# Performance work log

Measured on AMD Instinct MI355X. Metric: run time of the kernel, lower is better.

Reference implementation:

```python
import jax, jax.numpy as jnp
import numpy as np

N = 16384
K = 4096  # codebook_size
D = 512   # embedding_dim
COMMITMENT_COST = 0.25


def setup_inputs() -> dict:
    key = jax.random.key(0)
    kz, kc = jax.random.split(key)
    z = jax.random.normal(kz, (N, D), dtype=jnp.float32)
    # nn.Embedding weight init: uniform(-1/K, 1/K)
    codebook = jax.random.uniform(kc, (K, D), dtype=jnp.float32,
                                  minval=-1.0 / K, maxval=1.0 / K)
    return {"z": z, "codebook": codebook}


def reference(z, codebook):
    # squared L2 distances: [N, K]
    dists = (jnp.sum(z * z, axis=1, keepdims=True)
             + jnp.sum(codebook * codebook, axis=1)
             - 2.0 * jnp.matmul(z, codebook.T))
    idx = jnp.argmin(dists, axis=1)                 # [N]
    z_q = codebook[idx]                             # gather == one-hot @ codebook
    # straight-through estimator
    z_q_ste = z + jax.lax.stop_gradient(z_q - z)
    commitment_loss = jnp.mean((jax.lax.stop_gradient(z) - z_q) ** 2)
    codebook_loss = jnp.mean((z - jax.lax.stop_gradient(z_q)) ** 2)
    loss = codebook_loss + COMMITMENT_COST * commitment_loss
    encoding_indices = idx[:, None]                 # [N, 1] to match torch shape
    return (z_q_ste, encoding_indices, loss)
```

## Files before the change

kernel.cpp:

```cpp
#include <hip/hip_runtime.h>
#include <math.h>

#define N_ROWS 16384
#define K_CODES 4096
#define D_DIM 512
#define NCHUNK 8
#define KCHUNK (K_CODES / NCHUNK)
#define MARGIN 2.5e-3f

typedef unsigned int uint32;
typedef unsigned short u16t;
typedef __attribute__((ext_vector_type(8))) short short8;
typedef __attribute__((ext_vector_type(4))) float f32x4;

__device__ __forceinline__ float fmul_(float a, float b) { return __fmul_rn(a, b); }
__device__ __forceinline__ float fadd_(float a, float b) { return __fadd_rn(a, b); }

__device__ __forceinline__ u16t f2bf(float x) {
    uint32 u = __float_as_uint(x);
    return (u16t)((u + 0x7fffu + ((u >> 16) & 1u)) >> 16);
}
__device__ __forceinline__ float bf2f(u16t b) {
    return __uint_as_float(((uint32)b) << 16);
}

__global__ void rownorm_cvt_kernel(const float* __restrict__ src, int nrows,
                                   float* __restrict__ out,
                                   u16t* __restrict__ bf) {
    int gid = blockIdx.x * blockDim.x + threadIdx.x;
    int row = gid >> 2;
    int blk = gid & 3;
    if (row >= nrows) return;
    const size_t base = (size_t)row * D_DIM + blk * 128;
    const float4* p = (const float4*)(src + base);
    float4 v0 = p[0], v1 = p[1];
    if (bf) {
        ushort4 o0, o1;
        o0.x = f2bf(v0.x); o0.y = f2bf(v0.y); o0.z = f2bf(v0.z); o0.w = f2bf(v0.w);
        o1.x = f2bf(v1.x); o1.y = f2bf(v1.y); o1.z = f2bf(v1.z); o1.w = f2bf(v1.w);
        *(ushort4*)(bf + base) = o0;
        *(ushort4*)(bf + base + 4) = o1;
    }
    float r0 = fmul_(v0.x, v0.x), r1 = fmul_(v0.y, v0.y);
    float r2 = fmul_(v0.z, v0.z), r3 = fmul_(v0.w, v0.w);
    float r4 = fmul_(v1.x, v1.x), r5 = fmul_(v1.y, v1.y);
    float r6 = fmul_(v1.z, v1.z), r7 = fmul_(v1.w, v1.w);
#pragma unroll
    for (int i = 1; i < 16; i++) {
        float4 w0 = p[2 * i], w1 = p[2 * i + 1];
        if (bf) {
            ushort4 o0, o1;
            o0.x = f2bf(w0.x); o0.y = f2bf(w0.y); o0.z = f2bf(w0.z); o0.w = f2bf(w0.w);
            o1.x = f2bf(w1.x); o1.y = f2bf(w1.y); o1.z = f2bf(w1.z); o1.w = f2bf(w1.w);
            *(ushort4*)(bf + base + i * 8) = o0;
            *(ushort4*)(bf + base + i * 8 + 4) = o1;
        }
        r0 = fadd_(r0, fmul_(w0.x, w0.x));
        r1 = fadd_(r1, fmul_(w0.y, w0.y));
        r2 = fadd_(r2, fmul_(w0.z, w0.z));
        r3 = fadd_(r3, fmul_(w0.w, w0.w));
        r4 = fadd_(r4, fmul_(w1.x, w1.x));
        r5 = fadd_(r5, fmul_(w1.y, w1.y));
        r6 = fadd_(r6, fmul_(w1.z, w1.z));
        r7 = fadd_(r7, fmul_(w1.w, w1.w));
    }
    float s = fadd_(fadd_(fadd_(r0, r1), fadd_(r2, r3)),
                    fadd_(fadd_(r4, r5), fadd_(r6, r7)));
    float u = __shfl_down(s, 1, 64);
    float t = fadd_(s, u);
    float w = __shfl_down(t, 2, 64);
    float tot = fadd_(t, w);
    if (blk == 0) out[row] = tot;
}

#define STS 136

__global__ __launch_bounds__(256) void score_gemm_kernel(
    const u16t* __restrict__ zb, const u16t* __restrict__ cbb,
    const float* __restrict__ cnorm, u16t* __restrict__ scores) {
    __shared__ alignas(16) u16t Ab[128 * 32];
    __shared__ alignas(16) u16t Bb[128 * 32];
    __shared__ alignas(16) u16t stile[64 * STS];

    const int t = threadIdx.x;
    const int id = blockIdx.x;
    const int xcd = id & 7, q = id >> 3;
    const int bx = ((xcd & 3) << 1) | (q >> 6);
    const int by = ((xcd >> 2) << 6) | (q & 63);
    const int row0 = by * 128, k0 = bx * KCHUNK;
    const int w = t >> 6, lane = t & 63;
    const int wx = w & 1, wy = w >> 1;
    const int l15 = lane & 15, quad = lane >> 4;

    for (int kt = 0; kt < 4; kt++) {
        f32x4 acc[4][4];
#pragma unroll
        for (int i = 0; i < 4; i++)
#pragma unroll
            for (int j = 0; j < 4; j++) acc[i][j] = (f32x4){0.f, 0.f, 0.f, 0.f};

        for (int dt = 0; dt < 16; dt++) {
            __syncthreads();
#pragma unroll
            for (int qq = 0; qq < 2; qq++) {
                int s = qq * 256 + t;
                const u16t* ga = zb + (size_t)(row0 + (s >> 2)) * D_DIM + dt * 32 + (s & 3) * 8;
                __builtin_amdgcn_global_load_lds(
                    (const __attribute__((address_space(1))) void*)ga,
                    (__attribute__((address_space(3))) void*)((char*)Ab + qq * 4096 + w * 1024),
                    16, 0, 0);
                const u16t* gb = cbb + (size_t)(k0 + kt * 128 + (s >> 2)) * D_DIM + dt * 32 + (s & 3) * 8;
                __builtin_amdgcn_global_load_lds(
                    (const __attribute__((address_space(1))) void*)gb,
                    (__attribute__((address_space(3))) void*)((char*)Bb + qq * 4096 + w * 1024),
                    16, 0, 0);
            }
            __syncthreads();
            short8 a[4], b[4];
#pragma unroll
            for (int i = 0; i < 4; i++)
                a[i] = *(const short8*)((char*)Ab + (wy * 64 + i * 16 + l15) * 64 + quad * 16);
#pragma unroll
            for (int j = 0; j < 4; j++)
                b[j] = *(const short8*)((char*)Bb + (wx * 64 + j * 16 + l15) * 64 + quad * 16);
#pragma unroll
            for (int i = 0; i < 4; i++)
#pragma unroll
                for (int j = 0; j < 4; j++)
                    acc[i][j] = __builtin_amdgcn_mfma_f32_16x16x32_bf16(a[i], b[j], acc[i][j], 0, 0, 0);
        }
#pragma unroll
        for (int h = 0; h < 2; h++) {
            if (wy == h) {
#pragma unroll
                for (int j = 0; j < 4; j++) {
                    int cl = wx * 64 + j * 16 + l15;
                    float cn = cnorm[k0 + kt * 128 + cl];
#pragma unroll
                    for (int i = 0; i < 4; i++) {
#pragma unroll
                        for (int r = 0; r < 4; r++) {
                            int rl2 = i * 16 + quad * 4 + r;
                            float s = fmaf(-2.f, acc[i][j][r], cn);
                            stile[rl2 * STS + cl] = f2bf(s);
                        }
                    }
                }
            }
            __syncthreads();
            for (int idx = t; idx < 64 * 16; idx += 256) {
                int rr = idx >> 4, seg = idx & 15;
                short8 v = *(const short8*)&stile[rr * STS + seg * 8];
                *(short8*)(scores + (size_t)(row0 + h * 64 + rr) * K_CODES
                           + k0 + kt * 128 + seg * 8) = v;
            }
            __syncthreads();
        }
    }
}

__global__ __launch_bounds__(256) void scan_refine_wave_kernel(
    const u16t* __restrict__ scores,
    const float* __restrict__ z, const float* __restrict__ cb,
    const float* __restrict__ zz, const float* __restrict__ cnorm,
    float* __restrict__ out_zq, float* __restrict__ out_idx,
    float* __restrict__ rowsum) {
    const int t = threadIdx.x;
    const int w = t >> 6, lane = t & 63;
    const int row = blockIdx.x * 4 + w;

    const u16t* srow = scores + (size_t)row * K_CODES;
    short8 sv[8];
#pragma unroll
    for (int p = 0; p < 8; p++)
        sv[p] = *(const short8*)(srow + p * 512 + lane * 8);

    float m = 3.4e38f;
#pragma unroll
    for (int p = 0; p < 8; p++)
#pragma unroll
        for (int e = 0; e < 8; e++)
            m = fminf(m, bf2f((u16t)sv[p][e]));
#pragma unroll
    for (int off = 1; off < 64; off <<= 1)
        m = fminf(m, __shfl_xor(m, off, 64));
    const float thr = m + MARGIN;

    const float* zr = z + (size_t)row * D_DIM;
    float4 z0 = *(const float4*)(zr + lane * 8);
    float4 z1 = *(const float4*)(zr + lane * 8 + 4);
    const float zzr = zz[row];

    float bv = 3.4e38f;
    int bi = 0x7fffffff;
#pragma unroll
    for (int p = 0; p < 8; p++) {
        uint32 lm = 0u;
#pragma unroll
        for (int e = 0; e < 8; e++)
            if (bf2f((u16t)sv[p][e]) <= thr) lm |= (1u << e);
        unsigned long long act = __ballot(lm != 0u);
        while (act) {
            int src = __ffsll(act) - 1;
            act &= act - 1;
            uint32 mb = (uint32)__shfl((int)lm, src, 64);
            while (mb) {
                int e = __ffs(mb) - 1;
                mb &= mb - 1;
                int k = p * 512 + src * 8 + e;
                const float* cr = cb + (size_t)k * D_DIM;
                float4 c0 = *(const float4*)(cr + lane * 8);
                float4 c1 = *(const float4*)(cr + lane * 8 + 4);
                float d = fmul_(z0.x, c0.x);
                d = fmaf(z0.y, c0.y, d); d = fmaf(z0.z, c0.z, d); d = fmaf(z0.w, c0.w, d);
                d = fmaf(z1.x, c1.x, d); d = fmaf(z1.y, c1.y, d);
                d = fmaf(z1.z, c1.z, d); d = fmaf(z1.w, c1.w, d);
#pragma unroll
                for (int off = 1; off < 64; off <<= 1)
                    d = fadd_(d, __shfl_xor(d, off, 64));
                float dist = fmaf(-2.f, d, fadd_(zzr, cnorm[k]));
                if (dist < bv || (dist == bv && k < bi)) { bv = dist; bi = k; }
            }
        }
    }
    const float* cq = cb + (size_t)bi * D_DIM;
    float4 c0 = *(const float4*)(cq + lane * 8);
    float4 c1 = *(const float4*)(cq + lane * 8 + 4);
    float4 o0, o1;
    o0.x = fadd_(z0.x, __fsub_rn(c0.x, z0.x));
    o0.y = fadd_(z0.y, __fsub_rn(c0.y, z0.y));
    o0.z = fadd_(z0.z, __fsub_rn(c0.z, z0.z));
    o0.w = fadd_(z0.w, __fsub_rn(c0.w, z0.w));
    o1.x = fadd_(z1.x, __fsub_rn(c1.x, z1.x));
    o1.y = fadd_(z1.y, __fsub_rn(c1.y, z1.y));
    o1.z = fadd_(z1.z, __fsub_rn(c1.z, z1.z));
    o1.w = fadd_(z1.w, __fsub_rn(c1.w, z1.w));
    float* orow = out_zq + (size_t)row * D_DIM + lane * 8;
    *(float4*)(orow) = o0;
    *(float4*)(orow + 4) = o1;
    float dx0 = z0.x - c0.x, dy0 = z0.y - c0.y, dz0 = z0.z - c0.z, dw0 = z0.w - c0.w;
    float dx1 = z1.x - c1.x, dy1 = z1.y - c1.y, dz1 = z1.z - c1.z, dw1 = z1.w - c1.w;
    float s = dx0 * dx0 + dy0 * dy0 + dz0 * dz0 + dw0 * dw0
            + dx1 * dx1 + dy1 * dy1 + dz1 * dz1 + dw1 * dw1;
#pragma unroll
    for (int off = 32; off; off >>= 1) s += __shfl_down(s, off, 64);
    if (lane == 0) {
        rowsum[row] = s;
        out_idx[row] = (float)bi;
    }
}

__global__ void loss_kernel(const float* __restrict__ rowsum,
                            float* __restrict__ out_loss) {
    __shared__ float sm[256];
    float s = 0.f;
    for (int i = threadIdx.x; i < N_ROWS; i += 256) s += rowsum[i];
    sm[threadIdx.x] = s;
    __syncthreads();
    for (int st = 128; st; st >>= 1) {
        if (threadIdx.x < st) sm[threadIdx.x] += sm[threadIdx.x + st];
        __syncthreads();
    }
    if (threadIdx.x == 0)
        *out_loss = 1.25f * sm[0] / (float)(N_ROWS * D_DIM);
}

#define BM 128
#define BN 128
#define BK 16
#define TM 8
#define TN 8

__global__ __launch_bounds__(256, 4) void vq_argmin_kernel(
    const float* __restrict__ z, const float* __restrict__ cb,
    const float* __restrict__ zz, const float* __restrict__ cnorm,
    float* __restrict__ pval, int* __restrict__ pidx) {
    __shared__ float As[BK][BM + 4];
    __shared__ float Bs[BK][BN + 4];
    __shared__ float rv[BM][17];
    __shared__ int   ri[BM][17];

    const int bx = blockIdx.x;
    const int by = blockIdx.y;
    const int row0 = by * BM;
    const int k0 = bx * KCHUNK;
    const int t = threadIdx.x;
    const int tx = t & 15;
    const int ty = t >> 4;

    float minv[TM];
    int   mini[TM];
#pragma unroll
    for (int i = 0; i < TM; i++) { minv[i] = 3.4e38f; mini[i] = 0; }
    float zrow[TM];
#pragma unroll
    for (int i = 0; i < TM; i++) zrow[i] = zz[row0 + ty * TM + i];
    const int sr = t >> 1;
    const int sdq = (t & 1) * 8;

    for (int kt = 0; kt < KCHUNK / BN; kt++) {
        const int col0 = k0 + kt * BN;
        float acc[TM][TN];
#pragma unroll
        for (int i = 0; i < TM; i++)
#pragma unroll
            for (int j = 0; j < TN; j++) acc[i][j] = 0.f;
        for (int dt = 0; dt < D_DIM; dt += BK) {
            {
                const float* src = z + (size_t)(row0 + sr) * D_DIM + dt + sdq;
                float4 v0 = *(const float4*)(src);
                float4 v1 = *(const float4*)(src + 4);
                As[sdq + 0][sr] = v0.x; As[sdq + 1][sr] = v0.y;
                As[sdq + 2][sr] = v0.z; As[sdq + 3][sr] = v0.w;
                As[sdq + 4][sr] = v1.x; As[sdq + 5][sr] = v1.y;
                As[sdq + 6][sr] = v1.z; As[sdq + 7][sr] = v1.w;
                const float* srcb = cb + (size_t)(col0 + sr) * D_DIM + dt + sdq;
                float4 w0 = *(const float4*)(srcb);
                float4 w1 = *(const float4*)(srcb + 4);
                Bs[sdq + 0][sr] = w0.x; Bs[sdq + 1][sr] = w0.y;
                Bs[sdq + 2][sr] = w0.z; Bs[sdq + 3][sr] = w0.w;
                Bs[sdq + 4][sr] = w1.x; Bs[sdq + 5][sr] = w1.y;
                Bs[sdq + 6][sr] = w1.z; Bs[sdq + 7][sr] = w1.w;
            }
            __syncthreads();
#pragma unroll
            for (int d = 0; d < BK; d++) {
                float a[TM], b[TN];
#pragma unroll
                for (int i = 0; i < TM; i++) a[i] = As[d][ty * TM + i];
#pragma unroll
                for (int j = 0; j < TN; j++) b[j] = Bs[d][tx * TN + j];
#pragma unroll
                for (int i = 0; i < TM; i++)
#pragma unroll
                    for (int j = 0; j < TN; j++)
                        acc[i][j] = fmaf(a[i], b[j], acc[i][j]);
            }
            __syncthreads();
        }
#pragma unroll
        for (int j = 0; j < TN; j++) {
            const int col = col0 + tx * TN + j;
            const float cn = cnorm[col];
#pragma unroll
            for (int i = 0; i < TM; i++) {
                float s1 = fadd_(zrow[i], cn);
                float s = fmaf(-2.f, acc[i][j], s1);
                if (s < minv[i]) { minv[i] = s; mini[i] = col; }
            }
        }
    }
#pragma unroll
    for (int i = 0; i < TM; i++) {
        rv[ty * TM + i][tx] = minv[i];
        ri[ty * TM + i][tx] = mini[i];
    }
    __syncthreads();
    if (t < BM) {
        float bv = rv[t][0];
        int   bi = ri[t][0];
#pragma unroll
        for (int x = 1; x < 16; x++) {
            float v = rv[t][x]; int ii = ri[t][x];
            if (v < bv || (v == bv && ii < bi)) { bv = v; bi = ii; }
        }
        pval[(size_t)(row0 + t) * NCHUNK + bx] = bv;
        pidx[(size_t)(row0 + t) * NCHUNK + bx] = bi;
    }
}

__global__ void finalize_kernel(const float* __restrict__ z,
                                const float* __restrict__ cb,
                                const float* __restrict__ pval,
                                const int* __restrict__ pidx,
                                float* __restrict__ out_zq,
                                float* __restrict__ out_idx,
                                float* __restrict__ rowsum) {
    int row = (blockIdx.x * blockDim.x + threadIdx.x) >> 6;
    int lane = threadIdx.x & 63;
    if (row >= N_ROWS) return;
    float bv = pval[(size_t)row * NCHUNK];
    int   bi = pidx[(size_t)row * NCHUNK];
#pragma unroll
    for (int c = 1; c < NCHUNK; c++) {
        float v = pval[(size_t)row * NCHUNK + c];
        int  ii = pidx[(size_t)row * NCHUNK + c];
        if (v < bv || (v == bv && ii < bi)) { bv = v; bi = ii; }
    }
    const float4* zr = (const float4*)(z + (size_t)row * D_DIM);
    const float4* cr = (const float4*)(cb + (size_t)bi * D_DIM);
    float4* orow = (float4*)(out_zq + (size_t)row * D_DIM);
    float s = 0.f;
#pragma unroll
    for (int i = 0; i < 2; i++) {
        float4 zv = zr[i * 64 + lane];
        float4 cv = cr[i * 64 + lane];
        float4 o;
        o.x = fadd_(zv.x, __fsub_rn(cv.x, zv.x));
        o.y = fadd_(zv.y, __fsub_rn(cv.y, zv.y));
        o.z = fadd_(zv.z, __fsub_rn(cv.z, zv.z));
        o.w = fadd_(zv.w, __fsub_rn(cv.w, zv.w));
        orow[i * 64 + lane] = o;
        float dx = zv.x - cv.x, dy = zv.y - cv.y;
        float dz = zv.z - cv.z, dw = zv.w - cv.w;
        s += dx * dx + dy * dy + dz * dz + dw * dw;
    }
#pragma unroll
    for (int off = 32; off; off >>= 1) s += __shfl_down(s, off, 64);
    if (lane == 0) {
        rowsum[row] = s;
        out_idx[row] = (float)bi;
    }
}

extern "C" void kernel_launch(void* const* d_in, const int* in_sizes, int n_in,
                              void* d_out, int out_size, void* d_ws, size_t ws_size,
                              hipStream_t stream) {
    const float* z  = (const float*)d_in[0];
    const float* cb = (const float*)d_in[1];
    float* out      = (float*)d_out;
    float* out_zq   = out;
    float* out_idx  = out + (size_t)N_ROWS * D_DIM;
    float* out_loss = out_idx + N_ROWS;

    float* zz     = (float*)d_ws;
    float* cnorm  = zz + N_ROWS;
    float* rowsum = cnorm + K_CODES;
    u16t*  z_bf   = (u16t*)(rowsum + N_ROWS);
    u16t*  cb_bf  = z_bf + (size_t)N_ROWS * D_DIM;
    u16t*  scores = cb_bf + (size_t)K_CODES * D_DIM;
    const size_t WS_NEEDED = (size_t)(N_ROWS + K_CODES + N_ROWS) * 4
                           + (size_t)N_ROWS * D_DIM * 2
                           + (size_t)K_CODES * D_DIM * 2
                           + (size_t)N_ROWS * K_CODES * 2;

    if (ws_size >= WS_NEEDED) {
        rownorm_cvt_kernel<<<(N_ROWS * 4) / 256, 256, 0, stream>>>(z, N_ROWS, zz, z_bf);
        rownorm_cvt_kernel<<<(K_CODES * 4) / 256, 256, 0, stream>>>(cb, K_CODES, cnorm, cb_bf);

        score_gemm_kernel<<<NCHUNK * (N_ROWS / 128), 256, 0, stream>>>(z_bf, cb_bf, cnorm, scores);
        scan_refine_wave_kernel<<<N_ROWS / 4, 256, 0, stream>>>(scores, z, cb, zz, cnorm,
                                                                out_zq, out_idx, rowsum);
        loss_kernel<<<1, 256, 0, stream>>>(rowsum, out_loss);
    } else {
        float* pval = rowsum + N_ROWS;
        int*   pidx = (int*)(pval + (size_t)N_ROWS * NCHUNK);
        rownorm_cvt_kernel<<<(N_ROWS * 4) / 256, 256, 0, stream>>>(z, N_ROWS, zz, (u16t*)0);
        rownorm_cvt_kernel<<<(K_CODES * 4) / 256, 256, 0, stream>>>(cb, K_CODES, cnorm, (u16t*)0);
        dim3 g2(NCHUNK, N_ROWS / BM);
        vq_argmin_kernel<<<g2, 256, 0, stream>>>(z, cb, zz, cnorm, pval, pidx);
        finalize_kernel<<<N_ROWS / 4, 256, 0, stream>>>(z, cb, pval, pidx,
                                                        out_zq, out_idx, rowsum);
        loss_kernel<<<1, 256, 0, stream>>>(rowsum, out_loss);
    }
}
```

Measured before the change: 312.3 us.

## Replace full bf16 score matrix with per-tile candidate lists from GEMM epilogue

The GEMM epilogue no longer writes the full N×K bf16 score matrix. It now computes a per-row minimum for each 128-code tile in registers and shared memory, and records up to four near-minimum candidates plus a count. The refine kernel reads the 32 tile minima and re-checks only candidates within the margin, falling back to a full 128-code scan when a tile overflows. This removes a 128 MB score write and its read-back, at the cost of shared-memory atomics and extra syncs in the epilogue. The change also widens the K step to 64, drops the XCD-aware block remap, and splits bf16 conversion out of the norm kernel.

```diff
diff --git a/kernel.cpp b/kernel.cpp
--- a/kernel.cpp
+++ b/kernel.cpp
@@ -6,7 +6,9 @@
 #define D_DIM 512
 #define NCHUNK 8
 #define KCHUNK (K_CODES / NCHUNK)
+#define N_TILES 32
 #define MARGIN 2.5e-3f
+#define ENTSLACK 1.0e-4f
 
 typedef unsigned int uint32;
 typedef unsigned short u16t;
@@ -24,23 +26,14 @@
     return __uint_as_float(((uint32)b) << 16);
 }
 
-__global__ void rownorm_cvt_kernel(const float* __restrict__ src, int nrows,
-                                   float* __restrict__ out,
-                                   u16t* __restrict__ bf) {
+__global__ void rownorm_np_kernel(const float* __restrict__ src, int nrows,
+                                  float* __restrict__ out) {
     int gid = blockIdx.x * blockDim.x + threadIdx.x;
     int row = gid >> 2;
     int blk = gid & 3;
     if (row >= nrows) return;
-    const size_t base = (size_t)row * D_DIM + blk * 128;
-    const float4* p = (const float4*)(src + base);
+    const float4* p = (const float4*)(src + (size_t)row * D_DIM + blk * 128);
     float4 v0 = p[0], v1 = p[1];
-    if (bf) {
-        ushort4 o0, o1;
-        o0.x = f2bf(v0.x); o0.y = f2bf(v0.y); o0.z = f2bf(v0.z); o0.w = f2bf(v0.w);
-        o1.x = f2bf(v1.x); o1.y = f2bf(v1.y); o1.z = f2bf(v1.z); o1.w = f2bf(v1.w);
-        *(ushort4*)(bf + base) = o0;
-        *(ushort4*)(bf + base + 4) = o1;
-    }
     float r0 = fmul_(v0.x, v0.x), r1 = fmul_(v0.y, v0.y);
     float r2 = fmul_(v0.z, v0.z), r3 = fmul_(v0.w, v0.w);
     float r4 = fmul_(v1.x, v1.x), r5 = fmul_(v1.y, v1.y);
@@ -48,13 +41,6 @@
 #pragma unroll
     for (int i = 1; i < 16; i++) {
         float4 w0 = p[2 * i], w1 = p[2 * i + 1];
-        if (bf) {
-            ushort4 o0, o1;
-            o0.x = f2bf(w0.x); o0.y = f2bf(w0.y); o0.z = f2bf(w0.z); o0.w = f2bf(w0.w);
-            o1.x = f2bf(w1.x); o1.y = f2bf(w1.y); o1.z = f2bf(w1.z); o1.w = f2bf(w1.w);
-            *(ushort4*)(bf + base + i * 8) = o0;
-            *(ushort4*)(bf + base + i * 8 + 4) = o1;
-        }
         r0 = fadd_(r0, fmul_(w0.x, w0.x));
         r1 = fadd_(r1, fmul_(w0.y, w0.y));
         r2 = fadd_(r2, fmul_(w0.z, w0.z));
@@ -73,24 +59,37 @@
     if (blk == 0) out[row] = tot;
 }
 
-#define STS 136
-
-__global__ __launch_bounds__(256) void score_gemm_kernel(
+__global__ void cvt_bf16_kernel(const float* __restrict__ src,
+                                u16t* __restrict__ dst, int n4) {
+    int i = blockIdx.x * blockDim.x + threadIdx.x;
+    if (i >= n4) return;
+    float4 v = ((const float4*)src)[i];
+    ushort4 o;
+    o.x = f2bf(v.x); o.y = f2bf(v.y); o.z = f2bf(v.z); o.w = f2bf(v.w);
+    ((ushort4*)dst)[i] = o;
+}
+
+__global__ __launch_bounds__(256) void score_cand_gemm_kernel(
     const u16t* __restrict__ zb, const u16t* __restrict__ cbb,
-    const float* __restrict__ cnorm, u16t* __restrict__ scores) {
-    __shared__ alignas(16) u16t Ab[128 * 32];
-    __shared__ alignas(16) u16t Bb[128 * 32];
-    __shared__ alignas(16) u16t stile[64 * STS];
+    const float* __restrict__ cnorm,
+    float* __restrict__ tmin_g, uint32* __restrict__ tcnt_g,
+    uint32* __restrict__ tent_g) {
+    __shared__ alignas(16) u16t Ab[128 * 64];
+    __shared__ alignas(16) u16t Bb[128 * 64];
+    __shared__ float rmin2[2][128];
+    __shared__ float tminS[128];
+    __shared__ uint32 cntS[128];
+    __shared__ alignas(16) uint32 entS[128][4];
 
     const int t = threadIdx.x;
-    const int id = blockIdx.x;
-    const int xcd = id & 7, q = id >> 3;
-    const int bx = ((xcd & 3) << 1) | (q >> 6);
-    const int by = ((xcd >> 2) << 6) | (q & 63);
+    const int bx = blockIdx.x;
+    const int by = blockIdx.y;
     const int row0 = by * 128, k0 = bx * KCHUNK;
     const int w = t >> 6, lane = t & 63;
     const int wx = w & 1, wy = w >> 1;
     const int l15 = lane & 15, quad = lane >> 4;
+    const int srow8 = (lane >> 3);
+    const int scol = (lane & 7) * 8;
 
     for (int kt = 0; kt < 4; kt++) {
         f32x4 acc[4][4];
@@ -99,68 +98,103 @@
 #pragma unroll
             for (int j = 0; j < 4; j++) acc[i][j] = (f32x4){0.f, 0.f, 0.f, 0.f};
 
-        for (int dt = 0; dt < 16; dt++) {
+        for (int dt = 0; dt < 8; dt++) {
             __syncthreads();
 #pragma unroll
-            for (int qq = 0; qq < 2; qq++) {
-                int s = qq * 256 + t;
-                const u16t* ga = zb + (size_t)(row0 + (s >> 2)) * D_DIM + dt * 32 + (s & 3) * 8;
+            for (int q = 0; q < 4; q++) {
+                int rin = q * 32 + w * 8 + srow8;
+                const u16t* ga = zb + (size_t)(row0 + rin) * D_DIM + dt * 64 + scol;
                 __builtin_amdgcn_global_load_lds(
                     (const __attribute__((address_space(1))) void*)ga,
-                    (__attribute__((address_space(3))) void*)((char*)Ab + qq * 4096 + w * 1024),
+                    (__attribute__((address_space(3))) void*)((char*)Ab + q * 4096 + w * 1024),
                     16, 0, 0);
-                const u16t* gb = cbb + (size_t)(k0 + kt * 128 + (s >> 2)) * D_DIM + dt * 32 + (s & 3) * 8;
+                const u16t* gb = cbb + (size_t)(k0 + kt * 128 + rin) * D_DIM + dt * 64 + scol;
                 __builtin_amdgcn_global_load_lds(
                     (const __attribute__((address_space(1))) void*)gb,
-                    (__attribute__((address_space(3))) void*)((char*)Bb + qq * 4096 + w * 1024),
+                    (__attribute__((address_space(3))) void*)((char*)Bb + q * 4096 + w * 1024),
                     16, 0, 0);
             }
             __syncthreads();
-            short8 a[4], b[4];
-#pragma unroll
-            for (int i = 0; i < 4; i++)
-                a[i] = *(const short8*)((char*)Ab + (wy * 64 + i * 16 + l15) * 64 + quad * 16);
-#pragma unroll
-            for (int j = 0; j < 4; j++)
-                b[j] = *(const short8*)((char*)Bb + (wx * 64 + j * 16 + l15) * 64 + quad * 16);
-#pragma unroll
-            for (int i = 0; i < 4; i++)
+#pragma unroll
+            for (int kk = 0; kk < 2; kk++) {
+                short8 a[4], b[4];
+#pragma unroll
+                for (int i = 0; i < 4; i++)
+                    a[i] = *(const short8*)((char*)Ab + (wy * 64 + i * 16 + l15) * 128 + kk * 64 + quad * 16);
 #pragma unroll
                 for (int j = 0; j < 4; j++)
-                    acc[i][j] = __builtin_amdgcn_mfma_f32_16x16x32_bf16(a[i], b[j], acc[i][j], 0, 0, 0);
-        }
-#pragma unroll
-        for (int h = 0; h < 2; h++) {
-            if (wy == h) {
+                    b[j] = *(const short8*)((char*)Bb + (wx * 64 + j * 16 + l15) * 128 + kk * 64 + quad * 16);
+#pragma unroll
+                for (int i = 0; i < 4; i++)
+#pragma unroll
+                    for (int j = 0; j < 4; j++)
+                        acc[i][j] = __builtin_amdgcn_mfma_f32_16x16x32_bf16(a[i], b[j], acc[i][j], 0, 0, 0);
+            }
+        }
+        float cn[4];
+#pragma unroll
+        for (int j = 0; j < 4; j++)
+            cn[j] = cnorm[k0 + kt * 128 + wx * 64 + j * 16 + l15];
+
+        float rm[16];
+#pragma unroll
+        for (int i = 0; i < 4; i++)
+#pragma unroll
+            for (int r = 0; r < 4; r++) {
+                float m = 3.4e38f;
+#pragma unroll
+                for (int j = 0; j < 4; j++)
+                    m = fminf(m, fmaf(-2.f, acc[i][j][r], cn[j]));
+                rm[i * 4 + r] = m;
+            }
+#pragma unroll
+        for (int off = 1; off < 16; off <<= 1)
+#pragma unroll
+            for (int p = 0; p < 16; p++)
+                rm[p] = fminf(rm[p], __shfl_xor(rm[p], off, 64));
+        if (l15 == 0) {
+#pragma unroll
+            for (int p = 0; p < 16; p++)
+                rmin2[wx][wy * 64 + (p >> 2) * 16 + quad * 4 + (p & 3)] = rm[p];
+        }
+        __syncthreads();
+        if (t < 128) {
+            tminS[t] = fminf(rmin2[0][t], rmin2[1][t]);
+            cntS[t] = 0u;
+        }
+        __syncthreads();
+#pragma unroll
+        for (int i = 0; i < 4; i++)
+#pragma unroll
+            for (int r = 0; r < 4; r++) {
+                int rl = wy * 64 + i * 16 + quad * 4 + r;
+                float thrR = tminS[rl] + MARGIN;
 #pragma unroll
                 for (int j = 0; j < 4; j++) {
-                    int cl = wx * 64 + j * 16 + l15;
-                    float cn = cnorm[k0 + kt * 128 + cl];
-#pragma unroll
-                    for (int i = 0; i < 4; i++) {
-#pragma unroll
-                        for (int r = 0; r < 4; r++) {
-                            int rl2 = i * 16 + quad * 4 + r;
-                            float s = fmaf(-2.f, acc[i][j][r], cn);
-                            stile[rl2 * STS + cl] = f2bf(s);
+                    float s = fmaf(-2.f, acc[i][j][r], cn[j]);
+                    if (s <= thrR) {
+                        uint32 pos = atomicAdd(&cntS[rl], 1u);
+                        if (pos < 4u) {
+                            uint32 klocal = (uint32)(wx * 64 + j * 16 + l15);
+                            entS[rl][pos] = (klocal << 16) | (uint32)f2bf(s);
                         }
                     }
                 }
             }
-            __syncthreads();
-            for (int idx = t; idx < 64 * 16; idx += 256) {
-                int rr = idx >> 4, seg = idx & 15;
-                short8 v = *(const short8*)&stile[rr * STS + seg * 8];
-                *(short8*)(scores + (size_t)(row0 + h * 64 + rr) * K_CODES
-                           + k0 + kt * 128 + seg * 8) = v;
-            }
-            __syncthreads();
-        }
-    }
-}
-
-__global__ __launch_bounds__(256) void scan_refine_wave_kernel(
-    const u16t* __restrict__ scores,
+        __syncthreads();
+        if (t < 128) {
+            int ti = bx * 4 + kt;
+            size_t base = (size_t)ti * N_ROWS + row0 + t;
+            tmin_g[base] = tminS[t];
+            tcnt_g[base] = cntS[t];
+            *(uint4*)&tent_g[base * 4] = *(const uint4*)&entS[t][0];
+        }
+    }
+}
+
+__global__ __launch_bounds__(256) void refine2_kernel(
+    const float* __restrict__ tmin_g, const uint32* __restrict__ tcnt_g,
+    const uint32* __restrict__ tent_g,
     const float* __restrict__ z, const float* __restrict__ cb,
     const float* __restrict__ zz, const float* __restrict__ cnorm,
     float* __restrict__ out_zq, float* __restrict__ out_idx,
@@ -169,22 +203,13 @@
     const int w = t >> 6, lane = t & 63;
     const int row = blockIdx.x * 4 + w;
 
-    const u16t* srow = scores + (size_t)row * K_CODES;
-    short8 sv[8];
-#pragma unroll
-    for (int p = 0; p < 8; p++)
-        sv[p] = *(const short8*)(srow + p * 512 + lane * 8);
-
-    float m = 3.4e38f;
-#pragma unroll
-    for (int p = 0; p < 8; p++)
-#pragma unroll
-        for (int e = 0; e < 8; e++)
-            m = fminf(m, bf2f((u16t)sv[p][e]));
+    float tml = (lane < N_TILES) ? tmin_g[(size_t)lane * N_ROWS + row] : 3.4e38f;
+    float gm = tml;
 #pragma unroll
     for (int off = 1; off < 64; off <<= 1)
-        m = fminf(m, __shfl_xor(m, off, 64));
-    const float thr = m + MARGIN;
+        gm = fminf(gm, __shfl_xor(gm, off, 64));
+    const float gthrA = gm + MARGIN;
+    const float gthrB = gthrA + ENTSLACK;
 
     const float* zr = z + (size_t)row * D_DIM;
     float4 z0 = *(const float4*)(zr + lane * 8);
@@ -193,36 +218,42 @@
 
     float bv = 3.4e38f;
     int bi = 0x7fffffff;
-#pragma unroll
-    for (int p = 0; p < 8; p++) {
-        uint32 lm = 0u;
-#pragma unroll
-        for (int e = 0; e < 8; e++)
-            if (bf2f((u16t)sv[p][e]) <= thr) lm |= (1u << e);
-        unsigned long long act = __ballot(lm != 0u);
-        while (act) {
-            int src = __ffsll(act) - 1;
-            act &= act - 1;
-            uint32 mb = (uint32)__shfl((int)lm, src, 64);
-            while (mb) {
-                int e = __ffs(mb) - 1;
-                mb &= mb - 1;
-                int k = p * 512 + src * 8 + e;
-                const float* cr = cb + (size_t)k * D_DIM;
-                float4 c0 = *(const float4*)(cr + lane * 8);
-                float4 c1 = *(const float4*)(cr + lane * 8 + 4);
-                float d = fmul_(z0.x, c0.x);
-                d = fmaf(z0.y, c0.y, d); d = fmaf(z0.z, c0.z, d); d = fmaf(z0.w, c0.w, d);
-                d = fmaf(z1.x, c1.x, d); d = fmaf(z1.y, c1.y, d);
-                d = fmaf(z1.z, c1.z, d); d = fmaf(z1.w, c1.w, d);
-#pragma unroll
-                for (int off = 1; off < 64; off <<= 1)
-                    d = fadd_(d, __shfl_xor(d, off, 64));
-                float dist = fmaf(-2.f, d, fadd_(zzr, cnorm[k]));
-                if (dist < bv || (dist == bv && k < bi)) { bv = dist; bi = k; }
-            }
-        }
-    }
+
+    auto refine = [&](int k) {
+        const float* cr = cb + (size_t)k * D_DIM;
+        float4 c0 = *(const float4*)(cr + lane * 8);
+        float4 c1 = *(const float4*)(cr + lane * 8 + 4);
+        float d = fmul_(z0.x, c0.x);
+        d = fmaf(z0.y, c0.y, d); d = fmaf(z0.z, c0.z, d); d = fmaf(z0.w, c0.w, d);
+        d = fmaf(z1.x, c1.x, d); d = fmaf(z1.y, c1.y, d);
+        d = fmaf(z1.z, c1.z, d); d = fmaf(z1.w, c1.w, d);
+#pragma unroll
+        for (int off = 1; off < 64; off <<= 1)
+            d = fadd_(d, __shfl_xor(d, off, 64));
+        float dist = fmaf(-2.f, d, fadd_(zzr, cnorm[k]));
+        if (dist < bv || (dist == bv && k < bi)) { bv = dist; bi = k; }
+    };
+
+    for (int ti = 0; ti < N_TILES; ti++) {
+        float tmv = __shfl(tml, ti, 64);
+        if (tmv > gthrA) continue;
+        uint32 cnt = tcnt_g[(size_t)ti * N_ROWS + row];
+        if (cnt <= 4u) {
+            uint4 ev = *(const uint4*)&tent_g[((size_t)ti * N_ROWS + row) * 4];
+            uint32 e4[4] = {ev.x, ev.y, ev.z, ev.w};
+#pragma unroll
+            for (uint32 e = 0; e < 4u; e++) {
+                if (e < cnt) {
+                    uint32 v = e4[e];
+                    if (bf2f((u16t)(v & 0xffffu)) <= gthrB)
+                        refine(ti * 128 + (int)(v >> 16));
+                }
+            }
+        } else {
+            for (int kk = 0; kk < 128; kk++) refine(ti * 128 + kk);
+        }
+    }
+
     const float* cq = cb + (size_t)bi * D_DIM;
     float4 c0 = *(const float4*)(cq + lane * 8);
     float4 c1 = *(const float4*)(cq + lane * 8 + 4);
@@ -423,30 +454,37 @@
     float* out_idx  = out + (size_t)N_ROWS * D_DIM;
     float* out_loss = out_idx + N_ROWS;
 
-    float* zz     = (float*)d_ws;
-    float* cnorm  = zz + N_ROWS;
-    float* rowsum = cnorm + K_CODES;
-    u16t*  z_bf   = (u16t*)(rowsum + N_ROWS);
-    u16t*  cb_bf  = z_bf + (size_t)N_ROWS * D_DIM;
-    u16t*  scores = cb_bf + (size_t)K_CODES * D_DIM;
+    float*  zz     = (float*)d_ws;
+    float*  cnorm  = zz + N_ROWS;
+    float*  rowsum = cnorm + K_CODES;
+    u16t*   z_bf   = (u16t*)(rowsum + N_ROWS);
+    u16t*   cb_bf  = z_bf + (size_t)N_ROWS * D_DIM;
+    float*  tmin_g = (float*)(cb_bf + (size_t)K_CODES * D_DIM);
+    uint32* tcnt_g = (uint32*)(tmin_g + (size_t)N_TILES * N_ROWS);
+    uint32* tent_g = tcnt_g + (size_t)N_TILES * N_ROWS;
     const size_t WS_NEEDED = (size_t)(N_ROWS + K_CODES + N_ROWS) * 4
                            + (size_t)N_ROWS * D_DIM * 2
                            + (size_t)K_CODES * D_DIM * 2
-                           + (size_t)N_ROWS * K_CODES * 2;
+                           + (size_t)N_TILES * N_ROWS * (4 + 4 + 16);
 
     if (ws_size >= WS_NEEDED) {
-        rownorm_cvt_kernel<<<(N_ROWS * 4) / 256, 256, 0, stream>>>(z, N_ROWS, zz, z_bf);
-        rownorm_cvt_kernel<<<(K_CODES * 4) / 256, 256, 0, stream>>>(cb, K_CODES, cnorm, cb_bf);
-
-        score_gemm_kernel<<<NCHUNK * (N_ROWS / 128), 256, 0, stream>>>(z_bf, cb_bf, cnorm, scores);
-        scan_refine_wave_kernel<<<N_ROWS / 4, 256, 0, stream>>>(scores, z, cb, zz, cnorm,
-                                                                out_zq, out_idx, rowsum);
+        cvt_bf16_kernel<<<(N_ROWS * D_DIM / 4) / 256, 256, 0, stream>>>(z, z_bf, N_ROWS * D_DIM / 4);
+        cvt_bf16_kernel<<<(K_CODES * D_DIM / 4) / 256, 256, 0, stream>>>(cb, cb_bf, K_CODES * D_DIM / 4);
+        rownorm_np_kernel<<<(N_ROWS * 4) / 256, 256, 0, stream>>>(z, N_ROWS, zz);
+        rownorm_np_kernel<<<(K_CODES * 4) / 256, 256, 0, stream>>>(cb, K_CODES, cnorm);
+
+        dim3 g1(NCHUNK, N_ROWS / 128);
+        score_cand_gemm_kernel<<<g1, 256, 0, stream>>>(z_bf, cb_bf, cnorm,
+                                                       tmin_g, tcnt_g, tent_g);
+        refine2_kernel<<<N_ROWS / 4, 256, 0, stream>>>(tmin_g, tcnt_g, tent_g,
+                                                       z, cb, zz, cnorm,
+                                                       out_zq, out_idx, rowsum);
         loss_kernel<<<1, 256, 0, stream>>>(rowsum, out_loss);
     } else {
         float* pval = rowsum + N_ROWS;
         int*   pidx = (int*)(pval + (size_t)N_ROWS * NCHUNK);
-        rownorm_cvt_kernel<<<(N_ROWS * 4) / 256, 256, 0, stream>>>(z, N_ROWS, zz, (u16t*)0);
-        rownorm_cvt_kernel<<<(K_CODES * 4) / 256, 256, 0, stream>>>(cb, K_CODES, cnorm, (u16t*)0);
+        rownorm_np_kernel<<<(N_ROWS * 4) / 256, 256, 0, stream>>>(z, N_ROWS, zz);
+        rownorm_np_kernel<<<(K_CODES * 4) / 256, 256, 0, stream>>>(cb, K_CODES, cnorm);
         dim3 g2(NCHUNK, N_ROWS / BM);
         vq_argmin_kernel<<<g2, 256, 0, stream>>>(z, cb, zz, cnorm, pval, pidx);
         finalize_kernel<<<N_ROWS / 4, 256, 0, stream>>>(z, cb, pval, pidx,
```

New measurement: 424.1 us. +35.8%, slower.
